# Performance work log

Hardware: AMD Instinct MI355X
Metric: run time of the kernel (lower is better)

Reference implementation:

```python
import jax, jax.numpy as jnp
import numpy as np

CLIP_IN = 1e6
CLIP_OUT = 1e6


def setup_inputs() -> dict:
    key = jax.random.key(0)
    kx, kw = jax.random.split(key)
    x = jax.random.normal(kx, (16, 4096, 2048), dtype=jnp.float32)
    # Learnable Taylor coefficients, shape [order+1, 1], 'random' init (normal, stddev 0.05
    # like tf.random_normal_initializer default)
    w = jax.random.normal(kw, (9, 1), dtype=jnp.float32) * 0.05
    return {"x": x, "w": w}


def reference(x, w):
    # Faithful math: out = sum_{i=0..order} w[i] * x^i, evaluated with Horner's method
    # (same polynomial as the original concat-powers + matmul + reduce_sum).
    xc = jnp.clip(x, -CLIP_IN, CLIP_IN)
    coefs = w[:, 0]  # [order+1]
    order = coefs.shape[0] - 1
    out = jnp.full_like(xc, coefs[order])
    for i in range(order - 1, -1, -1):  # small fixed loop over polynomial degree
        out = out * xc + coefs[i]
    out = jnp.clip(out, -CLIP_OUT, CLIP_OUT)
    return out
```

## Files before the change

### kernel.cpp

```cpp
#include <hip/hip_runtime.h>

#define CLIP_IN  1000000.0f
#define CLIP_OUT 1000000.0f

__device__ __forceinline__ float horner9(float x, const float* __restrict__ c) {
    float xc = fminf(fmaxf(x, -CLIP_IN), CLIP_IN);
    float r = c[8];
    r = fmaf(r, xc, c[7]);
    r = fmaf(r, xc, c[6]);
    r = fmaf(r, xc, c[5]);
    r = fmaf(r, xc, c[4]);
    r = fmaf(r, xc, c[3]);
    r = fmaf(r, xc, c[2]);
    r = fmaf(r, xc, c[1]);
    r = fmaf(r, xc, c[0]);
    return fminf(fmaxf(r, -CLIP_OUT), CLIP_OUT);
}

__global__ __launch_bounds__(256) void TaylorActivation_77043123355716_kernel(
        const float4* __restrict__ x4,
        const float* __restrict__ w,
        float4* __restrict__ out4,
        long long n4) {
    float c[9];
#pragma unroll
    for (int i = 0; i < 9; ++i) c[i] = w[i];

    long long idx = (long long)blockIdx.x * blockDim.x + threadIdx.x;
    const long long stride = (long long)gridDim.x * blockDim.x;
    for (; idx < n4; idx += stride) {
        float4 v = x4[idx];
        float4 o;
        o.x = horner9(v.x, c);
        o.y = horner9(v.y, c);
        o.z = horner9(v.z, c);
        o.w = horner9(v.w, c);
        out4[idx] = o;
    }
}

__global__ void TaylorActivation_77043123355716_tail(
        const float* __restrict__ x,
        const float* __restrict__ w,
        float* __restrict__ out,
        long long start, long long n) {
    float c[9];
#pragma unroll
    for (int i = 0; i < 9; ++i) c[i] = w[i];
    long long i = start + threadIdx.x;
    if (i < n) out[i] = horner9(x[i], c);
}

extern "C" void kernel_launch(void* const* d_in, const int* in_sizes, int n_in,
                              void* d_out, int out_size, void* d_ws, size_t ws_size,
                              hipStream_t stream) {
    const float* x = (const float*)d_in[0];
    const float* w = (const float*)d_in[1];
    float* out = (float*)d_out;

    long long n = (long long)in_sizes[0];
    long long n4 = n >> 2;
    long long rem = n & 3;

    int block = 256;
    long long total_blocks = (n4 + block - 1) / block;
    int grid = (int)(total_blocks < 2048 ? (total_blocks > 0 ? total_blocks : 1) : 2048);

    TaylorActivation_77043123355716_kernel<<<grid, block, 0, stream>>>(
        (const float4*)x, w, (float4*)out, n4);

    if (rem) {
        TaylorActivation_77043123355716_tail<<<1, 64, 0, stream>>>(
            x, w, out, n4 << 2, n);
    }
}
```

Before: 209.5 us.

## Use one-tile-per-block kernel with 8x unrolled nontemporal vector loads and stores

Replaces the grid-stride loop over a fixed 2048-block grid with a launch of one block per 8x256 float4 tile. Each thread issues all eight loads up front, then computes, then stores, using nontemporal load and store builtins. A grid-stride tail kernel handles the leftover elements. The aim is more memory-level parallelism and less cache pollution on a purely bandwidth-bound streaming op, at the cost of many more blocks and higher register use per thread.

```diff
diff --git a/kernel.cpp b/kernel.cpp
--- a/kernel.cpp
+++ b/kernel.cpp
@@ -2,6 +2,8 @@
 
 #define CLIP_IN  1000000.0f
 #define CLIP_OUT 1000000.0f
+
+typedef float f32x4 __attribute__((ext_vector_type(4)));
 
 __device__ __forceinline__ float horner9(float x, const float* __restrict__ c) {
     float xc = fminf(fmaxf(x, -CLIP_IN), CLIP_IN);
@@ -17,29 +19,39 @@
     return fminf(fmaxf(r, -CLIP_OUT), CLIP_OUT);
 }
 
-__global__ __launch_bounds__(256) void TaylorActivation_77043123355716_kernel(
-        const float4* __restrict__ x4,
+constexpr int BLOCK  = 256;
+constexpr int UNROLL = 8;
+
+__global__ __launch_bounds__(BLOCK) void TaylorActivation_77043123355716_kernel(
+        const f32x4* __restrict__ x4,
         const float* __restrict__ w,
-        float4* __restrict__ out4,
-        long long n4) {
+        f32x4* __restrict__ out4) {
     float c[9];
 #pragma unroll
     for (int i = 0; i < 9; ++i) c[i] = w[i];
 
-    long long idx = (long long)blockIdx.x * blockDim.x + threadIdx.x;
-    const long long stride = (long long)gridDim.x * blockDim.x;
-    for (; idx < n4; idx += stride) {
-        float4 v = x4[idx];
-        float4 o;
-        o.x = horner9(v.x, c);
-        o.y = horner9(v.y, c);
-        o.z = horner9(v.z, c);
-        o.w = horner9(v.w, c);
-        out4[idx] = o;
+    long long base = (long long)blockIdx.x * (BLOCK * UNROLL) + threadIdx.x;
+
+    f32x4 v[UNROLL];
+#pragma unroll
+    for (int i = 0; i < UNROLL; ++i)
+        v[i] = __builtin_nontemporal_load(&x4[base + (long long)i * BLOCK]);
+
+    f32x4 o[UNROLL];
+#pragma unroll
+    for (int i = 0; i < UNROLL; ++i) {
+        o[i].x = horner9(v[i].x, c);
+        o[i].y = horner9(v[i].y, c);
+        o[i].z = horner9(v[i].z, c);
+        o[i].w = horner9(v[i].w, c);
     }
+
+#pragma unroll
+    for (int i = 0; i < UNROLL; ++i)
+        __builtin_nontemporal_store(o[i], &out4[base + (long long)i * BLOCK]);
 }
 
-__global__ void TaylorActivation_77043123355716_tail(
+__global__ __launch_bounds__(BLOCK) void TaylorActivation_77043123355716_tail(
         const float* __restrict__ x,
         const float* __restrict__ w,
         float* __restrict__ out,
@@ -47,8 +59,9 @@
     float c[9];
 #pragma unroll
     for (int i = 0; i < 9; ++i) c[i] = w[i];
-    long long i = start + threadIdx.x;
-    if (i < n) out[i] = horner9(x[i], c);
+    long long i = start + (long long)blockIdx.x * blockDim.x + threadIdx.x;
+    const long long stride = (long long)gridDim.x * blockDim.x;
+    for (; i < n; i += stride) out[i] = horner9(x[i], c);
 }
 
 extern "C" void kernel_launch(void* const* d_in, const int* in_sizes, int n_in,
@@ -58,19 +71,23 @@
     const float* w = (const float*)d_in[1];
     float* out = (float*)d_out;
 
-    long long n = (long long)in_sizes[0];
+    long long n  = (long long)in_sizes[0];
     long long n4 = n >> 2;
-    long long rem = n & 3;
+    const long long tile = (long long)BLOCK * UNROLL;
+    long long full_tiles = n4 / tile;
+    long long covered4   = full_tiles * tile;
 
-    int block = 256;
-    long long total_blocks = (n4 + block - 1) / block;
-    int grid = (int)(total_blocks < 2048 ? (total_blocks > 0 ? total_blocks : 1) : 2048);
+    if (full_tiles > 0) {
+        TaylorActivation_77043123355716_kernel<<<(int)full_tiles, BLOCK, 0, stream>>>(
+            (const f32x4*)x, w, (f32x4*)out);
+    }
 
-    TaylorActivation_77043123355716_kernel<<<grid, block, 0, stream>>>(
-        (const float4*)x, w, (float4*)out, n4);
-
-    if (rem) {
-        TaylorActivation_77043123355716_tail<<<1, 64, 0, stream>>>(
-            x, w, out, n4 << 2, n);
+    long long rem_start = covered4 << 2;
+    if (rem_start < n) {
+        long long rem = n - rem_start;
+        int blocks = (int)((rem + BLOCK - 1) / BLOCK);
+        if (blocks > 1024) blocks = 1024;
+        TaylorActivation_77043123355716_tail<<<blocks, BLOCK, 0, stream>>>(
+            x, w, out, rem_start, n);
     }
 }
```

After: 177.3 us. 15.4% less time.
